# Performance work log

Measured on AMD Instinct MI355X. Metric: run time of the kernel, lower is better.

The kernel has to match this reference:

```python
import jax, jax.numpy as jnp
import numpy as np

DIM = 1024
NUM_HEADS = 16
HEAD_DIM = DIM // NUM_HEADS
EPS = 1e-5


def layernorm(x, scale, bias):
    # LayerNorm over the last (head_dim) axis
    mu = jnp.mean(x, axis=-1, keepdims=True)
    var = jnp.var(x, axis=-1, keepdims=True)
    return (x - mu) * jax.lax.rsqrt(var + EPS) * scale + bias


def rope(q):
    # q: [B, H, S, Hd]; standard rotate-half RoPE over head_dim
    S, Hd = q.shape[-2], q.shape[-1]
    inv_freq = 1.0 / (10000.0 ** (jnp.arange(0, Hd, 2, dtype=jnp.float32) / Hd))
    ang = jnp.arange(S, dtype=jnp.float32)[:, None] * inv_freq  # [S, Hd/2]
    cos, sin = jnp.cos(ang), jnp.sin(ang)
    q1, q2 = jnp.split(q, 2, axis=-1)
    return jnp.concatenate([q1 * cos - q2 * sin, q1 * sin + q2 * cos], axis=-1)


def setup_inputs() -> dict:
    key = jax.random.key(0)
    ks = jax.random.split(key, 8)
    B, S, S_ctx = 4, 2048, 2048
    s = 0.02
    return {
        "x": jax.random.normal(ks[0], (B, S, DIM), dtype=jnp.float32),
        "context": jax.random.normal(ks[1], (B, S_ctx, DIM), dtype=jnp.float32),
        "q_w": jax.random.normal(ks[2], (DIM, DIM), dtype=jnp.float32) * s,
        "kv_w": jax.random.normal(ks[3], (DIM, 2 * DIM), dtype=jnp.float32) * s,
        "qn_scale": jnp.ones((HEAD_DIM,), jnp.float32),
        "qn_bias": jnp.zeros((HEAD_DIM,), jnp.float32),
        "kn_scale": jnp.ones((HEAD_DIM,), jnp.float32),
        "kn_bias": jnp.zeros((HEAD_DIM,), jnp.float32),
        "proj_w": jax.random.normal(ks[4], (DIM, DIM), dtype=jnp.float32) * s,
        "proj_b": jnp.zeros((DIM,), jnp.float32),
    }


def reference(x, context, q_w, kv_w, qn_scale, qn_bias, kn_scale, kn_bias, proj_w, proj_b):
    B, S, C = x.shape
    S_ctx = context.shape[1]
    H, Hd = NUM_HEADS, HEAD_DIM
    # projections (no bias: qkv_bias=False)
    q = (x @ q_w).reshape(B, S, H, Hd).transpose(0, 2, 1, 3)        # [B,H,S,Hd]
    kv = (context @ kv_w).reshape(B, S_ctx, 2, H, Hd)
    k = kv[:, :, 0].transpose(0, 2, 1, 3)                           # [B,H,Sc,Hd]
    v = kv[:, :, 1].transpose(0, 2, 1, 3)
    # per-head LayerNorm on q and k
    q = layernorm(q, qn_scale, qn_bias)
    k = layernorm(k, kn_scale, kn_bias)
    # RoPE on q only (as in the original forward)
    q = rope(q)
    # SDPA (eval path: no mask, no dropout)
    scale = 1.0 / jnp.sqrt(jnp.float32(Hd))
    logits = jnp.einsum("bhsd,bhtd->bhst", q, k) * scale
    attn = jax.nn.softmax(logits, axis=-1)
    out = jnp.einsum("bhst,bhtd->bhsd", attn, v)                    # [B,H,S,Hd]
    out = out.transpose(0, 2, 1, 3).reshape(B, S, C)
    return out @ proj_w + proj_b
```

## Files before the change

### kernel.cpp

```cpp
#include <hip/hip_runtime.h>
#include <hip/hip_bf16.h>


typedef short bf16x8 __attribute__((ext_vector_type(8)));
typedef float f32x4 __attribute__((ext_vector_type(4)));

__device__ __forceinline__ short f2s(float f) {
    __hip_bfloat16 h = __float2bfloat16(f);
    return __builtin_bit_cast(short, h);
}

__device__ __forceinline__ f32x4 mfma16(bf16x8 a, bf16x8 b, f32x4 c) {
    return __builtin_amdgcn_mfma_f32_16x16x32_bf16(a, b, c, 0, 0, 0);
}

__device__ __forceinline__ void gload16(short* lds, const short* g) {
    __builtin_amdgcn_global_load_lds((const __attribute__((address_space(1))) void*)g,
                                     (__attribute__((address_space(3))) void*)lds,
                                     16, 0, 0);
}

__device__ __forceinline__ void drain_barrier() {
    asm volatile("s_waitcnt vmcnt(0) lgkmcnt(0)" ::: "memory");
    __syncthreads();
}

__device__ __forceinline__ unsigned int fbits(float f) {
    return __builtin_bit_cast(unsigned int, f);
}

__global__ __launch_bounds__(256) void conv_to_bf16(const float* __restrict__ x,
                                                    const float* __restrict__ ctx,
                                                    short* __restrict__ xb,
                                                    short* __restrict__ cb) {
    const size_t NV = 2097152;
    size_t i = (size_t)blockIdx.x * 256 + threadIdx.x;
    const float4* src = (i < NV) ? (const float4*)x : (const float4*)ctx;
    short* dst = (i < NV) ? xb : cb;
    size_t idx = (i < NV) ? i : i - NV;
    float4 v = src[idx];
    short4 o;
    o.x = f2s(v.x); o.y = f2s(v.y); o.z = f2s(v.z); o.w = f2s(v.w);
    ((short4*)dst)[idx] = o;
}

__global__ __launch_bounds__(256) void transpose_weights(
    const float* __restrict__ q_w, const float* __restrict__ kv_w,
    const float* __restrict__ proj_w,
    short* __restrict__ WqT, short* __restrict__ WkvT, short* __restrict__ WpT) {
    __shared__ float t[32][33];
    const float* src; short* dst; int ld, coff;
    switch (blockIdx.z) {
        case 0:  src = q_w;    dst = WqT;                 ld = 1024; coff = 0;    break;
        case 1:  src = kv_w;   dst = WkvT;                ld = 2048; coff = 0;    break;
        case 2:  src = kv_w;   dst = WkvT + 1024 * 1024;  ld = 2048; coff = 1024; break;
        default: src = proj_w; dst = WpT;                 ld = 1024; coff = 0;    break;
    }
    int n0 = blockIdx.x * 32, k0 = blockIdx.y * 32;
    int tx = threadIdx.x & 31, ty = threadIdx.x >> 5;
    #pragma unroll
    for (int j = 0; j < 32; j += 8)
        t[ty + j][tx] = src[(size_t)(k0 + ty + j) * ld + coff + n0 + tx];
    __syncthreads();
    #pragma unroll
    for (int j = 0; j < 32; j += 8)
        dst[(size_t)(n0 + ty + j) * 1024 + k0 + tx] = f2s(t[tx][ty + j]);
}

template <int MODE>
__global__ __launch_bounds__(256) void gemm128(
    const short* __restrict__ A,
    const short* __restrict__ Bt,
    const float* __restrict__ ln_scale,
    const float* __restrict__ ln_bias,
    short* __restrict__ outB,
    short* __restrict__ outB2,
    float* __restrict__ outF,
    const float* __restrict__ bias_vec) {
    __shared__ short smem[24576];
    const int tid = threadIdx.x;
    const int w = tid >> 6, lane = tid & 63, quad = lane >> 4, l15 = lane & 15;
    const int wr = w & 1, wc = w >> 1;
    const int m0 = blockIdx.y * 128, n0 = blockIdx.x * 128;

    const int srow = lane >> 2, slot = lane & 3;
    const int kslot = (slot ^ ((srow >> 1) & 3)) * 8;
    const short* Ag0 = A + (size_t)(m0 + w * 32 + srow) * 1024 + kslot;
    const short* Ag1 = Ag0 + (size_t)16 * 1024;
    const short* Bg0 = Bt + (size_t)(n0 + w * 32 + srow) * 1024 + kslot;
    const short* Bg1 = Bg0 + (size_t)16 * 1024;
    short* Al = smem + w * 1024;
    short* Bl = smem + 4096 + w * 1024;

    f32x4 acc[4][4];
    #pragma unroll
    for (int r = 0; r < 4; r++)
        #pragma unroll
        for (int c = 0; c < 4; c++) acc[r][c] = f32x4{0.f, 0.f, 0.f, 0.f};

    const int rsw = (l15 >> 1) & 3;
    const int rch = (quad ^ rsw) * 8;

    gload16(Al,              Ag0);
    gload16(Al + 512,        Ag1);
    gload16(Bl,              Bg0);
    gload16(Bl + 512,        Bg1);
    gload16(Al + 8192,       Ag0 + 32);
    gload16(Al + 8192 + 512, Ag1 + 32);
    gload16(Bl + 8192,       Bg0 + 32);
    gload16(Bl + 8192 + 512, Bg1 + 32);
    asm volatile("s_waitcnt vmcnt(4) lgkmcnt(0)" ::: "memory");
    __builtin_amdgcn_s_barrier();

    int curo = 0;
    int pfo = 16384;
    #pragma unroll 1
    for (int t = 0; t < 32; t++) {
        if (t < 30) {
            const int k0 = (t + 2) * 32;
            gload16(Al + pfo,       Ag0 + k0);
            gload16(Al + pfo + 512, Ag1 + k0);
            gload16(Bl + pfo,       Bg0 + k0);
            gload16(Bl + pfo + 512, Bg1 + k0);
        }
        bf16x8 af[4], bfr[4];
        #pragma unroll
        for (int rt = 0; rt < 4; rt++)
            af[rt] = *(const bf16x8*)(smem + curo + (wr * 64 + rt * 16 + l15) * 32 + rch);
        #pragma unroll
        for (int ct = 0; ct < 4; ct++)
            bfr[ct] = *(const bf16x8*)(smem + curo + 4096 + (wc * 64 + ct * 16 + l15) * 32 + rch);
        #pragma unroll
        for (int rt = 0; rt < 4; rt++)
            #pragma unroll
            for (int ct = 0; ct < 4; ct++)
                acc[rt][ct] = mfma16(af[rt], bfr[ct], acc[rt][ct]);
        if (t < 30) {
            asm volatile("s_waitcnt vmcnt(4) lgkmcnt(0)" ::: "memory");
        } else {
            asm volatile("s_waitcnt vmcnt(0) lgkmcnt(0)" ::: "memory");
        }
        __builtin_amdgcn_s_barrier();
        curo += 8192; if (curo == 24576) curo = 0;
        pfo  += 8192; if (pfo  == 24576) pfo  = 0;
    }

    const bool vpath = (MODE == 1) && (n0 >= 1024);
    if constexpr (MODE == 0 || MODE == 1) {
        if (!vpath) {
            #pragma unroll
            for (int rt = 0; rt < 4; rt++) {
                #pragma unroll
                for (int i = 0; i < 4; i++) {
                    float s = acc[rt][0][i] + acc[rt][1][i] + acc[rt][2][i] + acc[rt][3][i];
                    float q = acc[rt][0][i] * acc[rt][0][i] + acc[rt][1][i] * acc[rt][1][i] +
                              acc[rt][2][i] * acc[rt][2][i] + acc[rt][3][i] * acc[rt][3][i];
                    #pragma unroll
                    for (int off = 1; off < 16; off <<= 1) {
                        s += __shfl_xor(s, off, 64);
                        q += __shfl_xor(q, off, 64);
                    }
                    float mu = s * (1.f / 64.f);
                    float var = q * (1.f / 64.f) - mu * mu;
                    float rs = rsqrtf(var + 1e-5f);
                    float vals[4];
                    #pragma unroll
                    for (int ct = 0; ct < 4; ct++) {
                        int hd = ct * 16 + l15;
                        vals[ct] = (acc[rt][ct][i] - mu) * rs * ln_scale[hd] + ln_bias[hd];
                    }
                    if constexpr (MODE == 0) {
                        int sp = (m0 + wr * 64 + rt * 16 + quad * 4 + i) & 2047;
                        #pragma unroll
                        for (int ct = 0; ct < 2; ct++) {
                            int hd1 = ct * 16 + l15;
                            float ang = (float)sp * exp2f((float)hd1 * (-13.287712379549449f / 32.f));
                            float sn, cs;
                            sincosf(ang, &sn, &cs);
                            float v1 = vals[ct], v2 = vals[ct + 2];
                            vals[ct]     = v1 * cs - v2 * sn;
                            vals[ct + 2] = v1 * sn + v2 * cs;
                        }
                    }
                    #pragma unroll
                    for (int ct = 0; ct < 4; ct++) acc[rt][ct][i] = vals[ct];
                }
            }
            drain_barrier();
            short* Csm = smem;
            #pragma unroll
            for (int rt = 0; rt < 4; rt++)
                #pragma unroll
                for (int ct = 0; ct < 4; ct++)
                    #pragma unroll
                    for (int i = 0; i < 4; i++)
                        Csm[(wr * 64 + rt * 16 + quad * 4 + i) * 132 + wc * 64 + ct * 16 + l15] =
                            f2s(acc[rt][ct][i]);
            drain_barrier();
            #pragma unroll
            for (int it = 0; it < 8; it++) {
                int row = it * 16 + (tid >> 4);
                int chunk = tid & 15;
                bf16x8 v = *(const bf16x8*)(Csm + row * 132 + chunk * 8);
                int hh = ((n0 & 1023) >> 6) + (chunk >> 3);
                int m = m0 + row, b = m >> 11, sp = m & 2047;
                *(bf16x8*)(outB + ((size_t)(b * 16 + hh) * 2048 + sp) * 64 + (chunk & 7) * 8) = v;
            }
        } else {
            const int b = m0 >> 11, h = ((n0 - 1024) >> 6) + wc;
            const int sp = (m0 & 2047) + wr * 64 + quad * 4;
            #pragma unroll
            for (int rt = 0; rt < 4; rt++)
                #pragma unroll
                for (int ct = 0; ct < 4; ct++) {
                    short4 pk;
                    pk.x = f2s(acc[rt][ct][0]); pk.y = f2s(acc[rt][ct][1]);
                    pk.z = f2s(acc[rt][ct][2]); pk.w = f2s(acc[rt][ct][3]);
                    int hd = ct * 16 + l15;
                    *(short4*)(outB2 + ((size_t)(b * 16 + h) * 64 + hd) * 2048 + sp + rt * 16) = pk;
                }
        }
    } else {
        #pragma unroll
        for (int rt = 0; rt < 4; rt++)
            #pragma unroll
            for (int i = 0; i < 4; i++) {
                size_t m = m0 + wr * 64 + rt * 16 + quad * 4 + i;
                #pragma unroll
                for (int ct = 0; ct < 4; ct++) {
                    int n = n0 + wc * 64 + ct * 16 + l15;
                    outF[m * 1024 + n] = acc[rt][ct][i] + bias_vec[n];
                }
            }
    }
}

__global__ __launch_bounds__(256, 3) void attn_kernel(
    const short* __restrict__ Q,
    const short* __restrict__ K,
    const short* __restrict__ V,
    short* __restrict__ AO) {
    __shared__ short smem[8192 + 8192 + 4 * 32 * 72];
    const int tid = threadIdx.x;
    const int w = tid >> 6, lane = tid & 63, quad = lane >> 4, l15 = lane & 15;
    const int bh = blockIdx.x, qt = blockIdx.y;
    const short* Qb = Q + (size_t)bh * 2048 * 64;
    const short* Kb = K + (size_t)bh * 2048 * 64;
    const short* Vb = V + (size_t)bh * 64 * 2048;
    short* Pw = smem + 16384 + w * 32 * 72;
    const int q0 = qt * 128 + w * 32;

    const int srow = lane >> 2, slot = lane & 3;
    const int sw = (slot ^ ((srow >> 1) & 3)) * 8;
    const short* Kg = Kb + (size_t)(w * 16 + srow) * 64 + sw;
    const short* Vg = Vb + (size_t)(w * 16 + srow) * 2048 + sw;
    short* Kl0 = smem + w * 512;
    short* Vl0 = smem + 8192 + w * 512;

    bf16x8 bq[2][2];
    #pragma unroll
    for (int nt = 0; nt < 2; nt++)
        #pragma unroll
        for (int ks = 0; ks < 2; ks++)
            bq[nt][ks] = *(const bf16x8*)(Qb + (size_t)(q0 + nt * 16 + l15) * 64 + ks * 32 + quad * 8);

    f32x4 acco[4][2];
    #pragma unroll
    for (int ct = 0; ct < 4; ct++)
        #pragma unroll
        for (int nt = 0; nt < 2; nt++) acco[ct][nt] = f32x4{0.f, 0.f, 0.f, 0.f};
    float lsum[2] = {0.f, 0.f};
    const int rsw = (l15 >> 1) & 3;
    const int rch = (quad ^ rsw) * 8;

    gload16(Kl0,        Kg);
    gload16(Kl0 + 2048, Kg + 32);
    gload16(Vl0,        Vg);
    gload16(Vl0 + 2048, Vg + 32);
    drain_barrier();

    #pragma unroll 1
    for (int t = 0; t < 32; t++) {
        const int cur = (t & 1) * 4096;
        if (t < 31) {
            const int nxt = 4096 - cur;
            const int sc = (t + 1) * 64;
            gload16(Kl0 + nxt,        Kg + sc * 64);
            gload16(Kl0 + nxt + 2048, Kg + sc * 64 + 32);
            gload16(Vl0 + nxt,        Vg + sc);
            gload16(Vl0 + nxt + 2048, Vg + sc + 32);
        }
        bf16x8 ak[4][2], av[4][2];
        #pragma unroll
        for (int mt = 0; mt < 4; mt++)
            #pragma unroll
            for (int ks = 0; ks < 2; ks++)
                ak[mt][ks] = *(const bf16x8*)(smem + cur + ks * 2048 + (mt * 16 + l15) * 32 + rch);
        #pragma unroll
        for (int ct = 0; ct < 4; ct++)
            #pragma unroll
            for (int ks = 0; ks < 2; ks++)
                av[ct][ks] = *(const bf16x8*)(smem + 8192 + cur + ks * 2048 + (ct * 16 + l15) * 32 + rch);

        #pragma unroll
        for (int mt = 0; mt < 4; mt++) {
            #pragma unroll
            for (int nt = 0; nt < 2; nt++) {
                f32x4 st = f32x4{0.f, 0.f, 0.f, 0.f};
                st = mfma16(ak[mt][0], bq[nt][0], st);
                st = mfma16(ak[mt][1], bq[nt][1], st);
                float e0 = __builtin_amdgcn_exp2f(st[0] * 0.1803368801f - 11.5415605f);
                float e1 = __builtin_amdgcn_exp2f(st[1] * 0.1803368801f - 11.5415605f);
                float e2 = __builtin_amdgcn_exp2f(st[2] * 0.1803368801f - 11.5415605f);
                float e3 = __builtin_amdgcn_exp2f(st[3] * 0.1803368801f - 11.5415605f);
                lsum[nt] += (e0 + e1) + (e2 + e3);
                unsigned int p01 = __builtin_amdgcn_perm(fbits(e1), fbits(e0), 0x07060302u);
                unsigned int p23 = __builtin_amdgcn_perm(fbits(e3), fbits(e2), 0x07060302u);
                uint2 pw;
                pw.x = p01; pw.y = p23;
                *(uint2*)(Pw + (nt * 16 + l15) * 72 + mt * 16 + quad * 4) = pw;
            }
        }
        asm volatile("" ::: "memory");
        bf16x8 bp[2][2];
        #pragma unroll
        for (int nt = 0; nt < 2; nt++)
            #pragma unroll
            for (int ks = 0; ks < 2; ks++)
                bp[nt][ks] = *(const bf16x8*)(Pw + (nt * 16 + l15) * 72 + ks * 32 + quad * 8);
        #pragma unroll
        for (int ct = 0; ct < 4; ct++)
            #pragma unroll
            for (int nt = 0; nt < 2; nt++)
                #pragma unroll
                for (int ks = 0; ks < 2; ks++)
                    acco[ct][nt] = mfma16(av[ct][ks], bp[nt][ks], acco[ct][nt]);
        drain_barrier();
    }

    #pragma unroll
    for (int nt = 0; nt < 2; nt++) {
        lsum[nt] += __shfl_xor(lsum[nt], 16, 64);
        lsum[nt] += __shfl_xor(lsum[nt], 32, 64);
    }
    const int b = bh >> 4, h = bh & 15;
    #pragma unroll
    for (int nt = 0; nt < 2; nt++) {
        float inv = 1.f / lsum[nt];
        int sq = q0 + nt * 16 + l15;
        #pragma unroll
        for (int ct = 0; ct < 4; ct++) {
            short4 pk;
            pk.x = f2s(acco[ct][nt][0] * inv); pk.y = f2s(acco[ct][nt][1] * inv);
            pk.z = f2s(acco[ct][nt][2] * inv); pk.w = f2s(acco[ct][nt][3] * inv);
            *(short4*)(AO + ((size_t)b * 2048 + sq) * 1024 + h * 64 + ct * 16 + quad * 4) = pk;
        }
    }
}

extern "C" void kernel_launch(void* const* d_in, const int* in_sizes, int n_in,
                              void* d_out, int out_size, void* d_ws, size_t ws_size,
                              hipStream_t stream) {
    (void)in_sizes; (void)n_in; (void)out_size; (void)ws_size;
    const float* x      = (const float*)d_in[0];
    const float* ctx    = (const float*)d_in[1];
    const float* q_w    = (const float*)d_in[2];
    const float* kv_w   = (const float*)d_in[3];
    const float* qn_s   = (const float*)d_in[4];
    const float* qn_b   = (const float*)d_in[5];
    const float* kn_s   = (const float*)d_in[6];
    const float* kn_b   = (const float*)d_in[7];
    const float* proj_w = (const float*)d_in[8];
    const float* proj_b = (const float*)d_in[9];
    float* out = (float*)d_out;

    char* ws = (char*)d_ws;
    const size_t MB = 1024 * 1024;
    short* xb   = (short*)(ws + 0 * MB);
    short* cb   = (short*)(ws + 16 * MB);
    short* Qb   = (short*)(ws + 32 * MB);
    short* Kb   = (short*)(ws + 48 * MB);
    short* Vt   = (short*)(ws + 64 * MB);
    short* AO   = (short*)(ws + 80 * MB);
    short* WqT  = (short*)(ws + 96 * MB);
    short* WkvT = (short*)(ws + 98 * MB);
    short* WpT  = (short*)(ws + 102 * MB);

    conv_to_bf16<<<16384, 256, 0, stream>>>(x, ctx, xb, cb);
    transpose_weights<<<dim3(32, 32, 4), 256, 0, stream>>>(q_w, kv_w, proj_w, WqT, WkvT, WpT);
    gemm128<0><<<dim3(8, 64), 256, 0, stream>>>(xb, WqT, qn_s, qn_b, Qb, nullptr, nullptr, nullptr);
    gemm128<1><<<dim3(16, 64), 256, 0, stream>>>(cb, WkvT, kn_s, kn_b, Kb, Vt, nullptr, nullptr);
    attn_kernel<<<dim3(64, 16), 256, 0, stream>>>(Qb, Kb, Vt, AO);
    gemm128<2><<<dim3(8, 64), 256, 0, stream>>>(AO, WpT, nullptr, nullptr, nullptr, nullptr, out, proj_b);
}
```

Measured before the change: 355.4 us.

## Process two query tiles per attention block and fold softmax scale into Q

Each attention block now handles two 128-row query tiles, separated by 1024 rows, against one shared stream of K/V tiles. This halves K/V global loads and LDS staging per unit of query work, at the cost of more registers, a larger P buffer in shared memory, occupancy dropping from 3 to 2 blocks per SM, and half as many blocks in the grid. The softmax scale is multiplied into Q in the projection epilogue, and the constant offset is dropped from the exponent, which removes an FMA per score. Without the offset, larger unnormalized exponentials go into the accumulators; the per-head LayerNorm should keep these bounded.

After: 329.6 us. 7.3% less time.

```diff
diff --git a/kernel.cpp b/kernel.cpp
--- a/kernel.cpp
+++ b/kernel.cpp
@@ -181,6 +181,8 @@
                             vals[ct]     = v1 * cs - v2 * sn;
                             vals[ct + 2] = v1 * sn + v2 * cs;
                         }
+                        #pragma unroll
+                        for (int ct = 0; ct < 4; ct++) vals[ct] *= 0.1803368801f;
                     }
                     #pragma unroll
                     for (int ct = 0; ct < 4; ct++) acc[rt][ct][i] = vals[ct];
@@ -235,20 +237,19 @@
     }
 }
 
-__global__ __launch_bounds__(256, 3) void attn_kernel(
+__global__ __launch_bounds__(256, 2) void attn_kernel(
     const short* __restrict__ Q,
     const short* __restrict__ K,
     const short* __restrict__ V,
     short* __restrict__ AO) {
-    __shared__ short smem[8192 + 8192 + 4 * 32 * 72];
+    __shared__ short smem[8192 + 8192 + 2 * 4 * 32 * 72];
     const int tid = threadIdx.x;
     const int w = tid >> 6, lane = tid & 63, quad = lane >> 4, l15 = lane & 15;
     const int bh = blockIdx.x, qt = blockIdx.y;
     const short* Qb = Q + (size_t)bh * 2048 * 64;
     const short* Kb = K + (size_t)bh * 2048 * 64;
     const short* Vb = V + (size_t)bh * 64 * 2048;
-    short* Pw = smem + 16384 + w * 32 * 72;
-    const int q0 = qt * 128 + w * 32;
+    const int q0g[2] = {qt * 128 + w * 32, (qt + 8) * 128 + w * 32};
 
     const int srow = lane >> 2, slot = lane & 3;
     const int sw = (slot ^ ((srow >> 1) & 3)) * 8;
@@ -257,19 +258,24 @@
     short* Kl0 = smem + w * 512;
     short* Vl0 = smem + 8192 + w * 512;
 
-    bf16x8 bq[2][2];
-    #pragma unroll
-    for (int nt = 0; nt < 2; nt++)
-        #pragma unroll
-        for (int ks = 0; ks < 2; ks++)
-            bq[nt][ks] = *(const bf16x8*)(Qb + (size_t)(q0 + nt * 16 + l15) * 64 + ks * 32 + quad * 8);
-
-    f32x4 acco[4][2];
-    #pragma unroll
-    for (int ct = 0; ct < 4; ct++)
-        #pragma unroll
-        for (int nt = 0; nt < 2; nt++) acco[ct][nt] = f32x4{0.f, 0.f, 0.f, 0.f};
-    float lsum[2] = {0.f, 0.f};
+    bf16x8 bq[2][2][2];
+    #pragma unroll
+    for (int g = 0; g < 2; g++)
+        #pragma unroll
+        for (int nt = 0; nt < 2; nt++)
+            #pragma unroll
+            for (int ks = 0; ks < 2; ks++)
+                bq[g][nt][ks] =
+                    *(const bf16x8*)(Qb + (size_t)(q0g[g] + nt * 16 + l15) * 64 + ks * 32 + quad * 8);
+
+    f32x4 acco[2][4][2];
+    #pragma unroll
+    for (int g = 0; g < 2; g++)
+        #pragma unroll
+        for (int ct = 0; ct < 4; ct++)
+            #pragma unroll
+            for (int nt = 0; nt < 2; nt++) acco[g][ct][nt] = f32x4{0.f, 0.f, 0.f, 0.f};
+    float lsum[2][2] = {{0.f, 0.f}, {0.f, 0.f}};
     const int rsw = (l15 >> 1) & 3;
     const int rch = (quad ^ rsw) * 8;
 
@@ -290,12 +296,39 @@
             gload16(Vl0 + nxt,        Vg + sc);
             gload16(Vl0 + nxt + 2048, Vg + sc + 32);
         }
-        bf16x8 ak[4][2], av[4][2];
+        bf16x8 ak[4][2];
         #pragma unroll
         for (int mt = 0; mt < 4; mt++)
             #pragma unroll
             for (int ks = 0; ks < 2; ks++)
                 ak[mt][ks] = *(const bf16x8*)(smem + cur + ks * 2048 + (mt * 16 + l15) * 32 + rch);
+
+        #pragma unroll
+        for (int g = 0; g < 2; g++) {
+            short* Pw = smem + 16384 + g * 9216 + w * 2304;
+            #pragma unroll
+            for (int mt = 0; mt < 4; mt++) {
+                #pragma unroll
+                for (int nt = 0; nt < 2; nt++) {
+                    f32x4 st = f32x4{0.f, 0.f, 0.f, 0.f};
+                    st = mfma16(ak[mt][0], bq[g][nt][0], st);
+                    st = mfma16(ak[mt][1], bq[g][nt][1], st);
+                    float e0 = __builtin_amdgcn_exp2f(st[0]);
+                    float e1 = __builtin_amdgcn_exp2f(st[1]);
+                    float e2 = __builtin_amdgcn_exp2f(st[2]);
+                    float e3 = __builtin_amdgcn_exp2f(st[3]);
+                    lsum[g][nt] += (e0 + e1) + (e2 + e3);
+                    unsigned int p01 = __builtin_amdgcn_perm(fbits(e1), fbits(e0), 0x07060302u);
+                    unsigned int p23 = __builtin_amdgcn_perm(fbits(e3), fbits(e2), 0x07060302u);
+                    uint2 pw;
+                    pw.x = p01; pw.y = p23;
+                    *(uint2*)(Pw + (nt * 16 + l15) * 72 + mt * 16 + quad * 4) = pw;
+                }
+            }
+        }
+        asm volatile("" ::: "memory");
+
+        bf16x8 av[4][2];
         #pragma unroll
         for (int ct = 0; ct < 4; ct++)
             #pragma unroll
@@ -303,59 +336,47 @@
                 av[ct][ks] = *(const bf16x8*)(smem + 8192 + cur + ks * 2048 + (ct * 16 + l15) * 32 + rch);
 
         #pragma unroll
-        for (int mt = 0; mt < 4; mt++) {
-            #pragma unroll
-            for (int nt = 0; nt < 2; nt++) {
-                f32x4 st = f32x4{0.f, 0.f, 0.f, 0.f};
-                st = mfma16(ak[mt][0], bq[nt][0], st);
-                st = mfma16(ak[mt][1], bq[nt][1], st);
-                float e0 = __builtin_amdgcn_exp2f(st[0] * 0.1803368801f - 11.5415605f);
-                float e1 = __builtin_amdgcn_exp2f(st[1] * 0.1803368801f - 11.5415605f);
-                float e2 = __builtin_amdgcn_exp2f(st[2] * 0.1803368801f - 11.5415605f);
-                float e3 = __builtin_amdgcn_exp2f(st[3] * 0.1803368801f - 11.5415605f);
-                lsum[nt] += (e0 + e1) + (e2 + e3);
-                unsigned int p01 = __builtin_amdgcn_perm(fbits(e1), fbits(e0), 0x07060302u);
-                unsigned int p23 = __builtin_amdgcn_perm(fbits(e3), fbits(e2), 0x07060302u);
-                uint2 pw;
-                pw.x = p01; pw.y = p23;
-                *(uint2*)(Pw + (nt * 16 + l15) * 72 + mt * 16 + quad * 4) = pw;
-            }
-        }
-        asm volatile("" ::: "memory");
-        bf16x8 bp[2][2];
-        #pragma unroll
-        for (int nt = 0; nt < 2; nt++)
-            #pragma unroll
-            for (int ks = 0; ks < 2; ks++)
-                bp[nt][ks] = *(const bf16x8*)(Pw + (nt * 16 + l15) * 72 + ks * 32 + quad * 8);
-        #pragma unroll
-        for (int ct = 0; ct < 4; ct++)
+        for (int g = 0; g < 2; g++) {
+            short* Pw = smem + 16384 + g * 9216 + w * 2304;
+            bf16x8 bp[2][2];
             #pragma unroll
             for (int nt = 0; nt < 2; nt++)
                 #pragma unroll
                 for (int ks = 0; ks < 2; ks++)
-                    acco[ct][nt] = mfma16(av[ct][ks], bp[nt][ks], acco[ct][nt]);
+                    bp[nt][ks] = *(const bf16x8*)(Pw + (nt * 16 + l15) * 72 + ks * 32 + quad * 8);
+            #pragma unroll
+            for (int ct = 0; ct < 4; ct++)
+                #pragma unroll
+                for (int nt = 0; nt < 2; nt++)
+                    #pragma unroll
+                    for (int ks = 0; ks < 2; ks++)
+                        acco[g][ct][nt] = mfma16(av[ct][ks], bp[nt][ks], acco[g][ct][nt]);
+        }
         drain_barrier();
     }
 
     #pragma unroll
-    for (int nt = 0; nt < 2; nt++) {
-        lsum[nt] += __shfl_xor(lsum[nt], 16, 64);
-        lsum[nt] += __shfl_xor(lsum[nt], 32, 64);
-    }
+    for (int g = 0; g < 2; g++)
+        #pragma unroll
+        for (int nt = 0; nt < 2; nt++) {
+            lsum[g][nt] += __shfl_xor(lsum[g][nt], 16, 64);
+            lsum[g][nt] += __shfl_xor(lsum[g][nt], 32, 64);
+        }
     const int b = bh >> 4, h = bh & 15;
     #pragma unroll
-    for (int nt = 0; nt < 2; nt++) {
-        float inv = 1.f / lsum[nt];
-        int sq = q0 + nt * 16 + l15;
-        #pragma unroll
-        for (int ct = 0; ct < 4; ct++) {
-            short4 pk;
-            pk.x = f2s(acco[ct][nt][0] * inv); pk.y = f2s(acco[ct][nt][1] * inv);
-            pk.z = f2s(acco[ct][nt][2] * inv); pk.w = f2s(acco[ct][nt][3] * inv);
-            *(short4*)(AO + ((size_t)b * 2048 + sq) * 1024 + h * 64 + ct * 16 + quad * 4) = pk;
-        }
-    }
+    for (int g = 0; g < 2; g++)
+        #pragma unroll
+        for (int nt = 0; nt < 2; nt++) {
+            float inv = 1.f / lsum[g][nt];
+            int sq = q0g[g] + nt * 16 + l15;
+            #pragma unroll
+            for (int ct = 0; ct < 4; ct++) {
+                short4 pk;
+                pk.x = f2s(acco[g][ct][nt][0] * inv); pk.y = f2s(acco[g][ct][nt][1] * inv);
+                pk.z = f2s(acco[g][ct][nt][2] * inv); pk.w = f2s(acco[g][ct][nt][3] * inv);
+                *(short4*)(AO + ((size_t)b * 2048 + sq) * 1024 + h * 64 + ct * 16 + quad * 4) = pk;
+            }
+        }
 }
 
 extern "C" void kernel_launch(void* const* d_in, const int* in_sizes, int n_in,
@@ -390,6 +411,6 @@
     transpose_weights<<<dim3(32, 32, 4), 256, 0, stream>>>(q_w, kv_w, proj_w, WqT, WkvT, WpT);
     gemm128<0><<<dim3(8, 64), 256, 0, stream>>>(xb, WqT, qn_s, qn_b, Qb, nullptr, nullptr, nullptr);
     gemm128<1><<<dim3(16, 64), 256, 0, stream>>>(cb, WkvT, kn_s, kn_b, Kb, Vt, nullptr, nullptr);
-    attn_kernel<<<dim3(64, 16), 256, 0, stream>>>(Qb, Kb, Vt, AO);
+    attn_kernel<<<dim3(64, 8), 256, 0, stream>>>(Qb, Kb, Vt, AO);
     gemm128<2><<<dim3(8, 64), 256, 0, stream>>>(AO, WpT, nullptr, nullptr, nullptr, nullptr, out, proj_b);
 }
```
